# Kernel optimization log

Measured on AMD Instinct MI355X. Metric: run time of the kernel, lower is better.

The kernel has to match this reference:

```python
import jax, jax.numpy as jnp
import numpy as np

WIN_H, WIN_W = 7, 7
NUM_HEADS = 16
DIM = 512
HEAD_DIM = DIM // NUM_HEADS
SCALE = HEAD_DIM ** -0.5


def rel_pos_index(h, w):
    # Faithful port of get_relative_position_index
    xx, yy = jnp.meshgrid(jnp.arange(h), jnp.arange(w), indexing='ij')
    coords = jnp.stack([yy, xx], axis=0).reshape(2, -1)  # (2, N)
    rel = coords[:, :, None] - coords[:, None, :]        # (2, N, N)
    return (rel[0] + h - 1) * (2 * w - 1) + (rel[1] + w - 1)  # (N, N)


def setup_inputs() -> dict:
    key = jax.random.key(0)
    ks = jax.random.split(key, 5)
    B_, N, C = 4096, WIN_H * WIN_W, DIM
    num_win = 64
    return {
        'x': jax.random.normal(ks[0], (B_, N, C), dtype=jnp.float32),
        'mask': jnp.zeros((num_win, N, N), dtype=jnp.float32),  # 0/-inf shift mask; zeros = no shift
        'qkv_w': jax.random.normal(ks[1], (C, 3 * C), dtype=jnp.float32) * 0.02,
        'qkv_b': jnp.zeros((3 * C,), dtype=jnp.float32),
        'proj_w': jax.random.normal(ks[2], (C, C), dtype=jnp.float32) * 0.02,
        'proj_b': jnp.zeros((C,), dtype=jnp.float32),
        'bias_table': jax.random.normal(ks[3], ((2 * WIN_H - 1) * (2 * WIN_W - 1), NUM_HEADS), dtype=jnp.float32) * 0.02,
    }


def reference(x, mask, qkv_w, qkv_b, proj_w, proj_b, bias_table):
    B_, N, C = x.shape
    H, hd = NUM_HEADS, HEAD_DIM
    qkv = x @ qkv_w + qkv_b                                  # (B_, N, 3C)
    qkv = qkv.reshape(B_, N, 3, H, hd).transpose(2, 0, 3, 1, 4)  # (3, B_, H, N, hd)
    q, k, v = qkv[0], qkv[1], qkv[2]
    q = q * jnp.asarray(SCALE, dtype=qkv.dtype)
    attn = jnp.einsum('bhnd,bhmd->bhnm', q, k)               # (B_, H, N, N)
    idx = rel_pos_index(WIN_H, WIN_W)                        # (N, N)
    bias = bias_table[idx].transpose(2, 0, 1)                # (H, N, N)
    attn = attn + bias
    num_win = mask.shape[0]
    attn = attn.reshape(B_ // num_win, num_win, H, N, N) + mask[None, :, None]
    attn = jax.nn.softmax(attn.reshape(B_, H, N, N), axis=-1)
    out = jnp.einsum('bhnm,bhmd->bhnd', attn, v)             # (B_, H, N, hd)
    out = out.transpose(0, 2, 1, 3).reshape(B_, N, C)
    return out @ proj_w + proj_b
```

## Files before the change

kernel.cpp:

```cpp
#include <hip/hip_runtime.h>
#include <stdint.h>

#define WIN_N 49
#define NH 16
#define HD 32
#define CDIM 512
#define NB 4096
#define M_ROWS (NB * WIN_N)
#define QKV_N 1536
#define SCALE_Q 0.17677669529663689f

typedef __attribute__((ext_vector_type(8))) short bf16x8;
typedef __attribute__((ext_vector_type(4))) float f32x4;

__device__ __forceinline__ unsigned short f2bf(float f) {
  unsigned int u = __float_as_uint(f);
  u += 0x7fff + ((u >> 16) & 1);
  return (unsigned short)(u >> 16);
}
__device__ __forceinline__ unsigned int pack2(float a, float b) {
  return (unsigned int)f2bf(a) | ((unsigned int)f2bf(b) << 16);
}

typedef const __attribute__((address_space(1))) unsigned int* gas1_t;
typedef __attribute__((address_space(3))) unsigned int* las3_t;
#define GL2LDS(g, l) __builtin_amdgcn_global_load_lds((gas1_t)(g), (las3_t)(l), 16, 0, 0)

__global__ void prep_weights(const float* __restrict__ qkv_w,
                             const float* __restrict__ proj_w,
                             unsigned short* __restrict__ wqkv_t,
                             unsigned short* __restrict__ wproj_t) {
  int i = blockIdx.x * blockDim.x + threadIdx.x;
  if (i < QKV_N * CDIM) {
    int n = i >> 9, k = i & 511;
    wqkv_t[i] = f2bf(qkv_w[k * QKV_N + n]);
  } else {
    int j = i - QKV_N * CDIM;
    if (j < CDIM * CDIM) {
      int n = j >> 9, k = j & 511;
      wproj_t[j] = f2bf(proj_w[k * CDIM + n]);
    }
  }
}

__global__ void conv_x(const float* __restrict__ x,
                       unsigned short* __restrict__ xb, int n8) {
  int i = blockIdx.x * blockDim.x + threadIdx.x;
  const int stride = gridDim.x * blockDim.x;
  for (; i < n8; i += stride) {
    const float4* p = (const float4*)(x + (size_t)i * 8);
    float4 a = p[0], b = p[1];
    *(uint4*)(xb + (size_t)i * 8) =
        make_uint4(pack2(a.x, a.y), pack2(a.z, a.w), pack2(b.x, b.y), pack2(b.z, b.w));
  }
}

template <bool OUT_F32>
__global__ __launch_bounds__(256) void gemm_bt(
    const unsigned short* __restrict__ A, int lda,
    const unsigned short* __restrict__ Bt,
    void* __restrict__ Cptr, int ldc,
    const float* __restrict__ bias,
    int K, int scale_cols, float scale) {
  __shared__ __align__(16) unsigned short SB[4][128 * 32];
  const int tid = threadIdx.x;

  const int gx = gridDim.x;
  const int nwg = gx * gridDim.y;
  int lin = blockIdx.y * gx + blockIdx.x;
  lin = (lin & 7) * (nwg >> 3) + (lin >> 3);
  const int bm = (lin / gx) * 128;
  const int bn = (lin % gx) * 128;

  const int lane = tid & 63, wid = tid >> 6;
  const int wm = (wid & 1) * 64, wn = (wid >> 1) * 64;
  const int quad = lane >> 4, l16 = lane & 15;
  const int r0 = tid >> 2;
  const int c0 = (tid & 3) * 8;

  const f32x4 fzero = {0.f, 0.f, 0.f, 0.f};
  f32x4 acc[4][4];
#pragma unroll
  for (int i = 0; i < 4; i++)
#pragma unroll
    for (int j = 0; j < 4; j++) acc[i][j] = fzero;

  const unsigned short* pA = A + (size_t)(bm + r0) * lda + c0;
  const unsigned short* pB = Bt + (size_t)(bn + r0) * K + c0;
  const size_t a64 = (size_t)64 * lda;
  const size_t b64 = (size_t)64 * K;
  const int woff = wid * 512;

#define STAGE(ab, bb, kk_)                              \
  do {                                                  \
    GL2LDS(pA + (kk_), SB[ab] + woff);                  \
    GL2LDS(pA + (kk_) + a64, SB[ab] + woff + 2048);     \
    GL2LDS(pB + (kk_), SB[bb] + woff);                  \
    GL2LDS(pB + (kk_) + b64, SB[bb] + woff + 2048);     \
  } while (0)

#define COMPUTE(ab, bb)                                                          \
  do {                                                                           \
    bf16x8 a[4], b[4];                                                           \
    _Pragma("unroll") for (int i = 0; i < 4; i++)                                \
        a[i] = *(const bf16x8*)&SB[ab][(wm + i * 16 + l16) * 32 + quad * 8];     \
    _Pragma("unroll") for (int i = 0; i < 4; i++)                                \
        b[i] = *(const bf16x8*)&SB[bb][(wn + i * 16 + l16) * 32 + quad * 8];     \
    _Pragma("unroll") for (int i = 0; i < 4; i++)                                \
        _Pragma("unroll") for (int j = 0; j < 4; j++)                            \
            acc[i][j] = __builtin_amdgcn_mfma_f32_16x16x32_bf16(a[i], b[j],      \
                                                                acc[i][j], 0, 0, 0); \
  } while (0)

  const int nt = K >> 5;
  STAGE(0, 1, 0);
  for (int t = 0; t < nt; t += 2) {
    __syncthreads();
    STAGE(2, 3, (t + 1) * 32);
    COMPUTE(0, 1);
    __syncthreads();
    if (t + 2 < nt) STAGE(0, 1, (t + 2) * 32);
    COMPUTE(2, 3);
  }
#undef STAGE
#undef COMPUTE

  if constexpr (OUT_F32) {
#pragma unroll
    for (int i = 0; i < 4; i++) {
      const int row = bm + wm + i * 16 + quad * 4;
#pragma unroll
      for (int j = 0; j < 4; j++) {
        const int col = bn + wn + j * 16 + l16;
        const float bv = bias[col];
#pragma unroll
        for (int r = 0; r < 4; r++)
          ((float*)Cptr)[(size_t)(row + r) * ldc + col] = acc[i][j][r] + bv;
      }
    }
  } else {
    unsigned short* Ct = &SB[0][0];
    __syncthreads();
#pragma unroll
    for (int i = 0; i < 4; i++) {
#pragma unroll
      for (int j = 0; j < 4; j++) {
        const int colg = bn + wn + j * 16 + l16;
        const float bv = bias[colg];
        const float sc = (colg < scale_cols) ? scale : 1.0f;
        const int coll = wn + j * 16 + l16;
#pragma unroll
        for (int r = 0; r < 4; r++) {
          const int rowl = wm + i * 16 + quad * 4 + r;
          Ct[rowl * 128 + coll] = f2bf((acc[i][j][r] + bv) * sc);
        }
      }
    }
    __syncthreads();
#pragma unroll
    for (int tt = 0; tt < 8; tt++) {
      const int row = tt * 16 + (tid >> 4);
      const int ce = (tid & 15) * 8;
      uint4 vv = *(const uint4*)&Ct[row * 128 + ce];
      *(uint4*)&((unsigned short*)Cptr)[(size_t)(bm + row) * ldc + bn + ce] = vv;
    }
  }
}

__global__ __launch_bounds__(256) void attn_mfma(
    unsigned short* __restrict__ qkv,
    const float* __restrict__ bias_table,
    const float* __restrict__ mask) {
  const int PS = 72;
  const int VS = 64;
  __shared__ __align__(16) unsigned short Pl_all[4][64 * 72];
  __shared__ __align__(16) unsigned short Vt_all[4][32 * 64];
  const int tid = threadIdx.x;
  const int wid = tid >> 6, lane = tid & 63;
  const int quad = lane >> 4, l16 = lane & 15;
  const int b = blockIdx.x;
  const int h = blockIdx.y * 4 + wid;
  unsigned short* Pl = Pl_all[wid];
  unsigned short* Vt = Vt_all[wid];
  const size_t row0 = (size_t)b * WIN_N;

  bf16x8 aq[4], bk[4];
#pragma unroll
  for (int i = 0; i < 4; i++) {
    size_t r = row0 + i * 16 + l16;
    if (r > (size_t)(M_ROWS - 1)) r = M_ROWS - 1;
    const unsigned short* pq = qkv + r * QKV_N + h * HD + quad * 8;
    aq[i] = *(const bf16x8*)pq;
    bk[i] = *(const bf16x8*)(pq + 512);
  }

  {
    const int m = lane;
    if (m < WIN_N) {
      const unsigned short* pv = qkv + (row0 + m) * QKV_N + 1024 + h * HD;
      uint4 tv[4];
      tv[0] = *(const uint4*)(pv + 0);
      tv[1] = *(const uint4*)(pv + 8);
      tv[2] = *(const uint4*)(pv + 16);
      tv[3] = *(const uint4*)(pv + 24);
      const unsigned short* tmp = (const unsigned short*)tv;
#pragma unroll
      for (int d = 0; d < 32; d++) Vt[d * VS + m] = tmp[d];
    } else {
#pragma unroll
      for (int d = 0; d < 32; d++) Vt[d * VS + m] = 0;
    }
  }

  const f32x4 fzero = {0.f, 0.f, 0.f, 0.f};
  f32x4 s[4][4];
#pragma unroll
  for (int i = 0; i < 4; i++)
#pragma unroll
    for (int j = 0; j < 4; j++)
      s[i][j] = __builtin_amdgcn_mfma_f32_16x16x32_bf16(aq[i], bk[j], fzero, 0, 0, 0);

  const float* mrow = mask + (size_t)(b & 63) * (WIN_N * WIN_N);
#pragma unroll
  for (int i = 0; i < 4; i++) {
#pragma unroll
    for (int r = 0; r < 4; r++) {
      const int t = i * 16 + quad * 4 + r;
      const int ti = t / 7, tj = t % 7;
      float v[4];
#pragma unroll
      for (int j = 0; j < 4; j++) {
        const int m = j * 16 + l16;
        float x = s[i][j][r];
        if (t < WIN_N && m < WIN_N) {
          const int mi = m / 7, mj = m % 7;
          const int idx = (tj - mj + 6) * 13 + (ti - mi + 6);
          x += bias_table[idx * NH + h] + mrow[t * WIN_N + m];
        }
        if (m >= WIN_N) x = -3.0e38f;
        v[j] = x;
      }
      float mx = fmaxf(fmaxf(v[0], v[1]), fmaxf(v[2], v[3]));
      mx = fmaxf(mx, __shfl_xor(mx, 1));
      mx = fmaxf(mx, __shfl_xor(mx, 2));
      mx = fmaxf(mx, __shfl_xor(mx, 4));
      mx = fmaxf(mx, __shfl_xor(mx, 8));
      float p[4];
      float sum = 0.f;
#pragma unroll
      for (int j = 0; j < 4; j++) {
        p[j] = __expf(v[j] - mx);
        sum += p[j];
      }
      sum += __shfl_xor(sum, 1);
      sum += __shfl_xor(sum, 2);
      sum += __shfl_xor(sum, 4);
      sum += __shfl_xor(sum, 8);
      const float inv = 1.0f / sum;
#pragma unroll
      for (int j = 0; j < 4; j++) Pl[t * PS + j * 16 + l16] = f2bf(p[j] * inv);
    }
  }
  __syncthreads();

  f32x4 o[4][2];
#pragma unroll
  for (int i = 0; i < 4; i++)
#pragma unroll
    for (int ni = 0; ni < 2; ni++) o[i][ni] = fzero;
#pragma unroll
  for (int ki = 0; ki < 2; ki++) {
    bf16x8 bv[2];
#pragma unroll
    for (int ni = 0; ni < 2; ni++)
      bv[ni] = *(const bf16x8*)&Vt[(ni * 16 + l16) * VS + ki * 32 + quad * 8];
#pragma unroll
    for (int i = 0; i < 4; i++) {
      bf16x8 ap = *(const bf16x8*)&Pl[(i * 16 + l16) * PS + ki * 32 + quad * 8];
#pragma unroll
      for (int ni = 0; ni < 2; ni++)
        o[i][ni] = __builtin_amdgcn_mfma_f32_16x16x32_bf16(ap, bv[ni], o[i][ni], 0, 0, 0);
    }
  }

#pragma unroll
  for (int i = 0; i < 4; i++) {
#pragma unroll
    for (int r = 0; r < 4; r++) {
      const int t = i * 16 + quad * 4 + r;
      if (t < WIN_N) {
        unsigned short* po = qkv + (row0 + t) * QKV_N + h * HD;
        po[l16] = f2bf(o[i][0][r]);
        po[16 + l16] = f2bf(o[i][1][r]);
      }
    }
  }
}

extern "C" void kernel_launch(void* const* d_in, const int* in_sizes, int n_in,
                              void* d_out, int out_size, void* d_ws, size_t ws_size,
                              hipStream_t stream) {
  const float* x = (const float*)d_in[0];
  const float* mask = (const float*)d_in[1];
  const float* qkv_w = (const float*)d_in[2];
  const float* qkv_b = (const float*)d_in[3];
  const float* proj_w = (const float*)d_in[4];
  const float* proj_b = (const float*)d_in[5];
  const float* bias_table = (const float*)d_in[6];
  float* out = (float*)d_out;

  unsigned short* qkvb = (unsigned short*)d_ws;
  unsigned short* wqkv_t = qkvb + (size_t)M_ROWS * QKV_N;
  unsigned short* wproj_t = wqkv_t + (size_t)QKV_N * CDIM;

  unsigned short* xb = (unsigned short*)d_out;

  prep_weights<<<4096, 256, 0, stream>>>(qkv_w, proj_w, wqkv_t, wproj_t);
  conv_x<<<2048, 256, 0, stream>>>(x, xb, (M_ROWS * CDIM) / 8);

  gemm_bt<false><<<dim3(QKV_N / 128, M_ROWS / 128), 256, 0, stream>>>(
      xb, CDIM, wqkv_t, qkvb, QKV_N, qkv_b, CDIM, 512, SCALE_Q);

  attn_mfma<<<dim3(NB, NH / 4), 256, 0, stream>>>(qkvb, bias_table, mask);

  gemm_bt<true><<<dim3(CDIM / 128, M_ROWS / 128), 256, 0, stream>>>(
      qkvb, QKV_N, wproj_t, out, CDIM, proj_b, CDIM, 0, 1.0f);
}
```

Before: 1.831 ms.

## Deepen GEMM pipeline to four LDS stages with explicit vmcnt waits

```diff
diff --git a/kernel.cpp b/kernel.cpp
--- a/kernel.cpp
+++ b/kernel.cpp
@@ -25,6 +25,14 @@
 typedef const __attribute__((address_space(1))) unsigned int* gas1_t;
 typedef __attribute__((address_space(3))) unsigned int* las3_t;
 #define GL2LDS(g, l) __builtin_amdgcn_global_load_lds((gas1_t)(g), (las3_t)(l), 16, 0, 0)
+
+#define VMW(n) asm volatile("s_waitcnt vmcnt(" #n ")" ::: "memory")
+#define BAR()                                   \
+  do {                                          \
+    __builtin_amdgcn_s_barrier();               \
+    __builtin_amdgcn_sched_barrier(0);          \
+    asm volatile("" ::: "memory");              \
+  } while (0)
 
 __global__ void prep_weights(const float* __restrict__ qkv_w,
                              const float* __restrict__ proj_w,
@@ -56,13 +64,14 @@
 }
 
 template <bool OUT_F32>
-__global__ __launch_bounds__(256) void gemm_bt(
+__global__ __launch_bounds__(256, 2) void gemm_bt(
     const unsigned short* __restrict__ A, int lda,
     const unsigned short* __restrict__ Bt,
     void* __restrict__ Cptr, int ldc,
     const float* __restrict__ bias,
     int K, int scale_cols, float scale) {
-  __shared__ __align__(16) unsigned short SB[4][128 * 32];
+  __shared__ __align__(16) unsigned short As[4][4096];
+  __shared__ __align__(16) unsigned short Bs[4][4096];
   const int tid = threadIdx.x;
 
   const int gx = gridDim.x;
@@ -75,8 +84,6 @@
   const int lane = tid & 63, wid = tid >> 6;
   const int wm = (wid & 1) * 64, wn = (wid >> 1) * 64;
   const int quad = lane >> 4, l16 = lane & 15;
-  const int r0 = tid >> 2;
-  const int c0 = (tid & 3) * 8;
 
   const f32x4 fzero = {0.f, 0.f, 0.f, 0.f};
   f32x4 acc[4][4];
@@ -85,43 +92,49 @@
 #pragma unroll
     for (int j = 0; j < 4; j++) acc[i][j] = fzero;
 
-  const unsigned short* pA = A + (size_t)(bm + r0) * lda + c0;
-  const unsigned short* pB = Bt + (size_t)(bn + r0) * K + c0;
-  const size_t a64 = (size_t)64 * lda;
-  const size_t b64 = (size_t)64 * K;
-  const int woff = wid * 512;
-
-#define STAGE(ab, bb, kk_)                              \
-  do {                                                  \
-    GL2LDS(pA + (kk_), SB[ab] + woff);                  \
-    GL2LDS(pA + (kk_) + a64, SB[ab] + woff + 2048);     \
-    GL2LDS(pB + (kk_), SB[bb] + woff);                  \
-    GL2LDS(pB + (kk_) + b64, SB[bb] + woff + 2048);     \
+  const int rS = tid & 127;
+  const int cS = (tid >> 7) * 8;
+  const unsigned short* pA0 = A + (size_t)(bm + rS) * lda + cS;
+  const unsigned short* pB0 = Bt + (size_t)(bn + rS) * K + cS;
+
+#define STAGE(bb, kk_)                                    \
+  do {                                                    \
+    GL2LDS(pA0 + (kk_), &As[bb][wid * 512]);              \
+    GL2LDS(pA0 + (kk_) + 16, &As[bb][2048 + wid * 512]);  \
+    GL2LDS(pB0 + (kk_), &Bs[bb][wid * 512]);              \
+    GL2LDS(pB0 + (kk_) + 16, &Bs[bb][2048 + wid * 512]);  \
   } while (0)
 
-#define COMPUTE(ab, bb)                                                          \
+#define COMPUTE(bb)                                                              \
   do {                                                                           \
+    const unsigned short* Ab = &As[bb][quad * 1024];                             \
+    const unsigned short* Bb = &Bs[bb][quad * 1024];                             \
     bf16x8 a[4], b[4];                                                           \
     _Pragma("unroll") for (int i = 0; i < 4; i++)                                \
-        a[i] = *(const bf16x8*)&SB[ab][(wm + i * 16 + l16) * 32 + quad * 8];     \
+        a[i] = *(const bf16x8*)&Ab[(wm + i * 16 + l16) * 8];                     \
     _Pragma("unroll") for (int i = 0; i < 4; i++)                                \
-        b[i] = *(const bf16x8*)&SB[bb][(wn + i * 16 + l16) * 32 + quad * 8];     \
+        b[i] = *(const bf16x8*)&Bb[(wn + i * 16 + l16) * 8];                     \
+    __builtin_amdgcn_s_setprio(1);                                               \
     _Pragma("unroll") for (int i = 0; i < 4; i++)                                \
         _Pragma("unroll") for (int j = 0; j < 4; j++)                            \
             acc[i][j] = __builtin_amdgcn_mfma_f32_16x16x32_bf16(a[i], b[j],      \
                                                                 acc[i][j], 0, 0, 0); \
+    __builtin_amdgcn_s_setprio(0);                                               \
   } while (0)
 
   const int nt = K >> 5;
-  STAGE(0, 1, 0);
-  for (int t = 0; t < nt; t += 2) {
-    __syncthreads();
-    STAGE(2, 3, (t + 1) * 32);
-    COMPUTE(0, 1);
-    __syncthreads();
-    if (t + 2 < nt) STAGE(0, 1, (t + 2) * 32);
-    COMPUTE(2, 3);
-  }
+  STAGE(0, 0);
+  STAGE(1, 32);
+  STAGE(2, 64);
+  for (int t = 0; t < nt - 3; ++t) {
+    VMW(8);
+    BAR();
+    STAGE((t + 3) & 3, (t + 3) * 32);
+    COMPUTE(t & 3);
+  }
+  VMW(8); BAR(); COMPUTE((nt - 3) & 3);
+  VMW(4); BAR(); COMPUTE((nt - 2) & 3);
+  VMW(0); BAR(); COMPUTE((nt - 1) & 3);
 #undef STAGE
 #undef COMPUTE
 
@@ -139,7 +152,7 @@
       }
     }
   } else {
-    unsigned short* Ct = &SB[0][0];
+    unsigned short* Ct = &As[0][0];
     __syncthreads();
 #pragma unroll
     for (int i = 0; i < 4; i++) {
@@ -316,7 +329,7 @@
   unsigned short* xb = (unsigned short*)d_out;
 
   prep_weights<<<4096, 256, 0, stream>>>(qkv_w, proj_w, wqkv_t, wproj_t);
-  conv_x<<<2048, 256, 0, stream>>>(x, xb, (M_ROWS * CDIM) / 8);
+  conv_x<<<4096, 256, 0, stream>>>(x, xb, (M_ROWS * CDIM) / 8);
 
   gemm_bt<false><<<dim3(QKV_N / 128, M_ROWS / 128), 256, 0, stream>>>(
       xb, CDIM, wqkv_t, qkvb, QKV_N, qkv_b, CDIM, 512, SCALE_Q);
```

Measured after the change: 2.132 ms. +16.4%, slower.

## Fuse fp32-to-bf16 conversion of x into QKV GEMM and swizzle LDS

Applied to the files above, without the earlier changes.

```diff
diff --git a/kernel.cpp b/kernel.cpp
--- a/kernel.cpp
+++ b/kernel.cpp
@@ -26,43 +26,35 @@
 typedef __attribute__((address_space(3))) unsigned int* las3_t;
 #define GL2LDS(g, l) __builtin_amdgcn_global_load_lds((gas1_t)(g), (las3_t)(l), 16, 0, 0)
 
-__global__ void prep_weights(const float* __restrict__ qkv_w,
-                             const float* __restrict__ proj_w,
-                             unsigned short* __restrict__ wqkv_t,
-                             unsigned short* __restrict__ wproj_t) {
-  int i = blockIdx.x * blockDim.x + threadIdx.x;
-  if (i < QKV_N * CDIM) {
-    int n = i >> 9, k = i & 511;
-    wqkv_t[i] = f2bf(qkv_w[k * QKV_N + n]);
-  } else {
-    int j = i - QKV_N * CDIM;
-    if (j < CDIM * CDIM) {
-      int n = j >> 9, k = j & 511;
-      wproj_t[j] = f2bf(proj_w[k * CDIM + n]);
-    }
-  }
-}
-
-__global__ void conv_x(const float* __restrict__ x,
-                       unsigned short* __restrict__ xb, int n8) {
-  int i = blockIdx.x * blockDim.x + threadIdx.x;
-  const int stride = gridDim.x * blockDim.x;
-  for (; i < n8; i += stride) {
-    const float4* p = (const float4*)(x + (size_t)i * 8);
-    float4 a = p[0], b = p[1];
-    *(uint4*)(xb + (size_t)i * 8) =
-        make_uint4(pack2(a.x, a.y), pack2(a.z, a.w), pack2(b.x, b.y), pack2(b.z, b.w));
-  }
-}
-
-template <bool OUT_F32>
+__global__ __launch_bounds__(256) void prep_w_t(const float* __restrict__ src,
+                                                unsigned short* __restrict__ dst,
+                                                int RS, int CS) {
+  __shared__ float T[64][65];
+  const int tid = threadIdx.x;
+  const int k0 = blockIdx.y * 64;
+  const int n0 = blockIdx.x * 64;
+  const int c = tid & 63;
+#pragma unroll
+  for (int rr = 0; rr < 16; rr++) {
+    const int row = rr * 4 + (tid >> 6);
+    T[row][c] = src[(size_t)(k0 + row) * CS + n0 + c];
+  }
+  __syncthreads();
+#pragma unroll
+  for (int wr = 0; wr < 16; wr++) {
+    const int n = wr * 4 + (tid >> 6);
+    dst[(size_t)(n0 + n) * RS + k0 + c] = f2bf(T[c][n]);
+  }
+}
+
+template <bool A_F32, bool OUT_F32>
 __global__ __launch_bounds__(256) void gemm_bt(
-    const unsigned short* __restrict__ A, int lda,
+    const void* __restrict__ Aptr, int lda,
     const unsigned short* __restrict__ Bt,
     void* __restrict__ Cptr, int ldc,
     const float* __restrict__ bias,
     int K, int scale_cols, float scale) {
-  __shared__ __align__(16) unsigned short SB[4][128 * 32];
+  __shared__ __align__(16) unsigned short SB[4][4096];
   const int tid = threadIdx.x;
 
   const int gx = gridDim.x;
@@ -75,8 +67,7 @@
   const int lane = tid & 63, wid = tid >> 6;
   const int wm = (wid & 1) * 64, wn = (wid >> 1) * 64;
   const int quad = lane >> 4, l16 = lane & 15;
-  const int r0 = tid >> 2;
-  const int c0 = (tid & 3) * 8;
+  const int sRd = quad ^ ((l16 >> 1) & 3);
 
   const f32x4 fzero = {0.f, 0.f, 0.f, 0.f};
   f32x4 acc[4][4];
@@ -85,27 +76,60 @@
 #pragma unroll
     for (int j = 0; j < 4; j++) acc[i][j] = fzero;
 
-  const unsigned short* pA = A + (size_t)(bm + r0) * lda + c0;
-  const unsigned short* pB = Bt + (size_t)(bn + r0) * K + c0;
+  const int rS = tid >> 2;
+  const int sS = (tid & 3) ^ ((tid >> 3) & 3);
+  const float* pAf = (const float*)Aptr + (size_t)(bm + rS) * lda + sS * 8;
+  const unsigned short* pAb = (const unsigned short*)Aptr + (size_t)(bm + rS) * lda + sS * 8;
+  const unsigned short* pB0 = Bt + (size_t)(bn + rS) * K + sS * 8;
   const size_t a64 = (size_t)64 * lda;
   const size_t b64 = (size_t)64 * K;
-  const int woff = wid * 512;
-
-#define STAGE(ab, bb, kk_)                              \
-  do {                                                  \
-    GL2LDS(pA + (kk_), SB[ab] + woff);                  \
-    GL2LDS(pA + (kk_) + a64, SB[ab] + woff + 2048);     \
-    GL2LDS(pB + (kk_), SB[bb] + woff);                  \
-    GL2LDS(pB + (kk_) + b64, SB[bb] + woff + 2048);     \
+  const int dsA0 = rS * 32 + (tid & 3) * 8;
+  const int dsA1 = (rS + 64) * 32 + (tid & 3) * 8;
+
+  float4 ax0, ax1, ay0, ay1;
+
+#define LOADREG(kk_)                          \
+  do {                                        \
+    if constexpr (A_F32) {                    \
+      const float* p = pAf + (kk_);           \
+      ax0 = *(const float4*)p;                \
+      ax1 = *(const float4*)(p + 4);          \
+      ay0 = *(const float4*)(p + a64);        \
+      ay1 = *(const float4*)(p + a64 + 4);    \
+    }                                         \
+  } while (0)
+
+#define DSWRITE_A(ab)                                                            \
+  do {                                                                           \
+    if constexpr (A_F32) {                                                       \
+      *(uint4*)&SB[ab][dsA0] = make_uint4(pack2(ax0.x, ax0.y), pack2(ax0.z, ax0.w), \
+                                          pack2(ax1.x, ax1.y), pack2(ax1.z, ax1.w)); \
+      *(uint4*)&SB[ab][dsA1] = make_uint4(pack2(ay0.x, ay0.y), pack2(ay0.z, ay0.w), \
+                                          pack2(ay1.x, ay1.y), pack2(ay1.z, ay1.w)); \
+    }                                                                            \
+  } while (0)
+
+#define STAGE_AB16(ab, kk_)                               \
+  do {                                                    \
+    if constexpr (!A_F32) {                               \
+      GL2LDS(pAb + (kk_), &SB[ab][wid * 512]);            \
+      GL2LDS(pAb + (kk_) + a64, &SB[ab][2048 + wid * 512]); \
+    }                                                     \
+  } while (0)
+
+#define STAGE_B(bb, kk_)                                  \
+  do {                                                    \
+    GL2LDS(pB0 + (kk_), &SB[bb][wid * 512]);              \
+    GL2LDS(pB0 + (kk_) + b64, &SB[bb][2048 + wid * 512]); \
   } while (0)
 
 #define COMPUTE(ab, bb)                                                          \
   do {                                                                           \
     bf16x8 a[4], b[4];                                                           \
     _Pragma("unroll") for (int i = 0; i < 4; i++)                                \
-        a[i] = *(const bf16x8*)&SB[ab][(wm + i * 16 + l16) * 32 + quad * 8];     \
+        a[i] = *(const bf16x8*)&SB[ab][(wm + i * 16 + l16) * 32 + sRd * 8];      \
     _Pragma("unroll") for (int i = 0; i < 4; i++)                                \
-        b[i] = *(const bf16x8*)&SB[bb][(wn + i * 16 + l16) * 32 + quad * 8];     \
+        b[i] = *(const bf16x8*)&SB[bb][(wn + i * 16 + l16) * 32 + sRd * 8];      \
     _Pragma("unroll") for (int i = 0; i < 4; i++)                                \
         _Pragma("unroll") for (int j = 0; j < 4; j++)                            \
             acc[i][j] = __builtin_amdgcn_mfma_f32_16x16x32_bf16(a[i], b[j],      \
@@ -113,16 +137,24 @@
   } while (0)
 
   const int nt = K >> 5;
-  STAGE(0, 1, 0);
+  LOADREG(0);
+  STAGE_AB16(0, 0);
+  STAGE_B(1, 0);
+  DSWRITE_A(0);
   for (int t = 0; t < nt; t += 2) {
     __syncthreads();
-    STAGE(2, 3, (t + 1) * 32);
+    if (t + 1 < nt) { LOADREG((t + 1) * 32); STAGE_AB16(2, (t + 1) * 32); STAGE_B(3, (t + 1) * 32); }
     COMPUTE(0, 1);
+    if (t + 1 < nt) DSWRITE_A(2);
     __syncthreads();
-    if (t + 2 < nt) STAGE(0, 1, (t + 2) * 32);
+    if (t + 2 < nt) { LOADREG((t + 2) * 32); STAGE_AB16(0, (t + 2) * 32); STAGE_B(1, (t + 2) * 32); }
     COMPUTE(2, 3);
-  }
-#undef STAGE
+    if (t + 2 < nt) DSWRITE_A(0);
+  }
+#undef LOADREG
+#undef DSWRITE_A
+#undef STAGE_AB16
+#undef STAGE_B
 #undef COMPUTE
 
   if constexpr (OUT_F32) {
@@ -283,16 +315,21 @@
     }
   }
 
-#pragma unroll
-  for (int i = 0; i < 4; i++) {
-#pragma unroll
-    for (int r = 0; r < 4; r++) {
-      const int t = i * 16 + quad * 4 + r;
-      if (t < WIN_N) {
-        unsigned short* po = qkv + (row0 + t) * QKV_N + h * HD;
-        po[l16] = f2bf(o[i][0][r]);
-        po[16 + l16] = f2bf(o[i][1][r]);
-      }
+  unsigned short* Ol = Pl;
+#pragma unroll
+  for (int i = 0; i < 4; i++)
+#pragma unroll
+    for (int ni = 0; ni < 2; ni++)
+#pragma unroll
+      for (int r = 0; r < 4; r++)
+        Ol[(i * 16 + quad * 4 + r) * 32 + ni * 16 + l16] = f2bf(o[i][ni][r]);
+#pragma unroll
+  for (int p = 0; p < 4; p++) {
+    const int row = p * 16 + (lane >> 2);
+    if (row < WIN_N) {
+      const int ce = (lane & 3) * 8;
+      uint4 vv = *(const uint4*)&Ol[row * 32 + ce];
+      *(uint4*)(qkv + (row0 + row) * QKV_N + h * HD + ce) = vv;
     }
   }
 }
@@ -313,16 +350,14 @@
   unsigned short* wqkv_t = qkvb + (size_t)M_ROWS * QKV_N;
   unsigned short* wproj_t = wqkv_t + (size_t)QKV_N * CDIM;
 
-  unsigned short* xb = (unsigned short*)d_out;
-
-  prep_weights<<<4096, 256, 0, stream>>>(qkv_w, proj_w, wqkv_t, wproj_t);
-  conv_x<<<2048, 256, 0, stream>>>(x, xb, (M_ROWS * CDIM) / 8);
-
-  gemm_bt<false><<<dim3(QKV_N / 128, M_ROWS / 128), 256, 0, stream>>>(
-      xb, CDIM, wqkv_t, qkvb, QKV_N, qkv_b, CDIM, 512, SCALE_Q);
+  prep_w_t<<<dim3(QKV_N / 64, CDIM / 64), 256, 0, stream>>>(qkv_w, wqkv_t, CDIM, QKV_N);
+  prep_w_t<<<dim3(CDIM / 64, CDIM / 64), 256, 0, stream>>>(proj_w, wproj_t, CDIM, CDIM);
+
+  gemm_bt<true, false><<<dim3(QKV_N / 128, M_ROWS / 128), 256, 0, stream>>>(
+      x, CDIM, wqkv_t, qkvb, QKV_N, qkv_b, CDIM, 512, SCALE_Q);
 
   attn_mfma<<<dim3(NB, NH / 4), 256, 0, stream>>>(qkvb, bias_table, mask);
 
-  gemm_bt<true><<<dim3(CDIM / 128, M_ROWS / 128), 256, 0, stream>>>(
+  gemm_bt<false, true><<<dim3(CDIM / 128, M_ROWS / 128), 256, 0, stream>>>(
       qkvb, QKV_N, wproj_t, out, CDIM, proj_b, CDIM, 0, 1.0f);
 }
```

After: 2.643 ms. 44.3% more time.
